# Optimization experiments

Measured on AMD Instinct MI355X. Metric: run time of the kernel, lower is better.

The kernel has to match this reference:

```python
import jax, jax.numpy as jnp
import numpy as np
from jax import lax

TARGETED_NUM_POINTS = 2000


def fps_indices(pts, m):
    """Furthest-point sampling indices for one cloud. pts: [n,3] -> [m] int32.
    Matches pointnet2_utils.furthest_point_sample: first index is 0, then
    iteratively pick the point with max distance to the selected set."""
    n = pts.shape[0]

    def step(carry, _):
        dist, last = carry
        d = jnp.sum((pts - pts[last]) ** 2, axis=-1)  # [n]
        dist = jnp.minimum(dist, d)
        nxt = jnp.argmax(dist).astype(jnp.int32)
        return (dist, nxt), nxt

    dist0 = jnp.full((n,), 1e10, dtype=pts.dtype)
    (_, _), idxs = lax.scan(step, (dist0, jnp.int32(0)), None, length=m - 1)
    return jnp.concatenate([jnp.zeros((1,), jnp.int32), idxs])


def setup_inputs() -> dict:
    key = jax.random.key(0)
    k1, k2 = jax.random.split(key)
    batch, n_pts, c = 8, 20000, 128
    return {
        "input_C": jax.random.normal(k1, (batch * n_pts, 3), dtype=jnp.float32),
        "input_F": jax.random.normal(k2, (batch * n_pts, c), dtype=jnp.float32),
        "batch": batch,
        "n_pts": n_pts,
    }


def reference(input_C, input_F, batch, n_pts):
    # pts_list = [n_pts]*batch (equal-size clouds), so the flat tensors reshape cleanly.
    C = input_C.reshape(batch, n_pts, 3)
    F = input_F.reshape(batch, n_pts, -1)
    m = min(TARGETED_NUM_POINTS, n_pts)
    idxs = jax.vmap(lambda p: fps_indices(p, m))(C)  # [b, m]
    sampled_C = jnp.take_along_axis(C, idxs[..., None], axis=1)  # [b, m, 3]
    sampled_F = jnp.take_along_axis(F, idxs[..., None], axis=1)  # [b, m, c]
    return sampled_C, sampled_F
```

## Files before the change

### kernel.cpp

```cpp
#include <hip/hip_runtime.h>
#include <hip/hip_bf16.h>

typedef unsigned long long ull;

#define THREADS 1024
#define NWAVE 16

template<int CTRL, int RM>
__device__ __forceinline__ float fmax_dpp(float v) {
    int s = __builtin_amdgcn_update_dpp(__float_as_int(v), __float_as_int(v), CTRL, RM, 0xf, false);
    return fmaxf(v, __int_as_float(s));
}
template<int CTRL, int RM>
__device__ __forceinline__ float fmin_dpp(float v) {
    int s = __builtin_amdgcn_update_dpp(__float_as_int(v), __float_as_int(v), CTRL, RM, 0xf, false);
    return fminf(v, __int_as_float(s));
}
template<int CTRL, int RM>
__device__ __forceinline__ int imin_dpp(int v) {
    int s = __builtin_amdgcn_update_dpp(v, v, CTRL, RM, 0xf, false);
    return (s < v) ? s : v;
}
template<int CTRL, int RM>
__device__ __forceinline__ ull kmax_dpp(ull k) {
    unsigned hi = (unsigned)(k >> 32), lo = (unsigned)k;
    unsigned hi2 = (unsigned)__builtin_amdgcn_update_dpp((int)hi, (int)hi, CTRL, RM, 0xf, false);
    unsigned lo2 = (unsigned)__builtin_amdgcn_update_dpp((int)lo, (int)lo, CTRL, RM, 0xf, false);
    ull k2 = ((ull)hi2 << 32) | lo2;
    return (k2 > k) ? k2 : k;
}
__device__ __forceinline__ float wave_fmax(float v) {
    v = fmax_dpp<0x111,0xf>(v); v = fmax_dpp<0x112,0xf>(v);
    v = fmax_dpp<0x114,0xf>(v); v = fmax_dpp<0x118,0xf>(v);
    v = fmax_dpp<0x142,0xa>(v); v = fmax_dpp<0x143,0xc>(v);
    return v;
}
__device__ __forceinline__ float wave_fmin(float v) {
    v = fmin_dpp<0x111,0xf>(v); v = fmin_dpp<0x112,0xf>(v);
    v = fmin_dpp<0x114,0xf>(v); v = fmin_dpp<0x118,0xf>(v);
    v = fmin_dpp<0x142,0xa>(v); v = fmin_dpp<0x143,0xc>(v);
    return v;
}
__device__ __forceinline__ float half_fmax(float v) {
    v = fmax_dpp<0x111,0xf>(v); v = fmax_dpp<0x112,0xf>(v);
    v = fmax_dpp<0x114,0xf>(v); v = fmax_dpp<0x118,0xf>(v);
    v = fmax_dpp<0x142,0xa>(v);
    return v;
}
__device__ __forceinline__ float half_fmin(float v) {
    v = fmin_dpp<0x111,0xf>(v); v = fmin_dpp<0x112,0xf>(v);
    v = fmin_dpp<0x114,0xf>(v); v = fmin_dpp<0x118,0xf>(v);
    v = fmin_dpp<0x142,0xa>(v);
    return v;
}
__device__ __forceinline__ int half_imin(int v) {
    v = imin_dpp<0x111,0xf>(v); v = imin_dpp<0x112,0xf>(v);
    v = imin_dpp<0x114,0xf>(v); v = imin_dpp<0x118,0xf>(v);
    v = imin_dpp<0x142,0xa>(v);
    return v;
}
__device__ __forceinline__ ull wave_kmax(ull k) {
    k = kmax_dpp<0x111,0xf>(k); k = kmax_dpp<0x112,0xf>(k);
    k = kmax_dpp<0x114,0xf>(k); k = kmax_dpp<0x118,0xf>(k);
    k = kmax_dpp<0x142,0xa>(k); k = kmax_dpp<0x143,0xc>(k);
    return k;
}
__device__ __forceinline__ int morton4(int x, int y, int z) {
    int r = 0;
#pragma unroll
    for (int k = 0; k < 4; ++k)
        r |= ((x >> k & 1) << (3 * k)) | ((y >> k & 1) << (3 * k + 1)) | ((z >> k & 1) << (3 * k + 2));
    return r;
}
__device__ __forceinline__ int cellof(float x, float y, float z,
                                      float bx, float by, float bz,
                                      float ivx, float ivy, float ivz) {
    int ix = (int)((x - bx) * ivx); ix = ix < 0 ? 0 : (ix > 15 ? 15 : ix);
    int iy = (int)((y - by) * ivy); iy = iy < 0 ? 0 : (iy > 15 ? 15 : iy);
    int iz = (int)((z - bz) * ivz); iz = iz < 0 ? 0 : (iz > 15 ? 15 : iz);
    return morton4(ix, iy, iz);
}

#define OFS_GKEY 0
#define OFS_GWIN 8192
#define OFS_GMAX 24576
#define OFS_CX   28672
#define OFS_CY   32768
#define OFS_CZ   36864
#define OFS_EX   40960
#define OFS_EY   45056
#define OFS_EZ   49152
#define OFS_LIST 53248
#define OFS_PART 55296
#define OFS_MISC 55552
#define OFS_RED  55680
#define FIXED_BYTES 56064

__device__ __forceinline__ void phaseC(
    const float4* __restrict__ gx, float* __restrict__ s_dist,
    ull* __restrict__ s_gkey, float* __restrict__ s_gmax,
    float4* __restrict__ s_gwin,
    const unsigned short* __restrict__ lst, int U,
    int lane, int half, int sub, int wid,
    float lx, float ly, float lz)
{
    const int nt = (U + 1) >> 1;
    int j = wid;
    if (j >= nt) return;
    int e = 2 * j + half;
    bool a = (e < U);
    int g = a ? (int)lst[e] : 0;
    int o = g * 32 + sub;
    float4 w = gx[o];
    while (j < nt) {
        const int jn = j + NWAVE;
        const int en = 2 * jn + half;
        bool an = (jn < nt) && (en < U);
        int gn = an ? (int)lst[en] : 0;
        int on = gn * 32 + sub;
        float4 wn = gx[on];
        float dc = a ? s_dist[o] : -1.0f;
        float dx = __fsub_rn(w.x, lx);
        float dy = __fsub_rn(w.y, ly);
        float dz = __fsub_rn(w.z, lz);
        float d  = __fadd_rn(__fadd_rn(__fmul_rn(dx, dx), __fmul_rn(dy, dy)),
                             __fmul_rn(dz, dz));
        float nd = fminf(dc, d);
        if (a) s_dist[o] = nd;
        float gm = __shfl(half_fmax(nd), lane | 31);
        int pk = (nd == gm) ? (int)w.w : 0x7FFFFFFF;
        int minorig = __shfl(half_imin(pk), lane | 31);
        if (a && nd == gm && (int)w.w == minorig)
            s_gwin[g] = w;
        if (a && sub == 31) {
            s_gkey[g] = ((ull)__float_as_uint(gm) << 25)
                      | ((ull)(unsigned)(0x7fff - minorig) << 10)
                      | (ull)(unsigned)g;
            s_gmax[g] = gm;
        }
        j = jn; a = an; g = gn; o = on; w = wn;
    }
}

__global__ __launch_bounds__(THREADS)
void fps_grouped(const float* __restrict__ C, float4* __restrict__ gxyzo,
                 int n, int m, int G32, int* __restrict__ idx_out) {
    const int b = blockIdx.x;
    const int t = threadIdx.x;
    const int lane = t & 63;
    const int wid  = t >> 6;
    const int half = lane >> 5;
    const int sub  = lane & 31;
    const int GP = G32 * 32;
    const float* __restrict__ P = C + (size_t)b * n * 3;
    float4* __restrict__ gx = gxyzo + (size_t)b * GP;

    extern __shared__ char smem[];
    ull*    s_gkey = (ull*)(smem + OFS_GKEY);
    float4* s_gwin = (float4*)(smem + OFS_GWIN);
    float*  s_gmax = (float*)(smem + OFS_GMAX);
    float*  s_cx   = (float*)(smem + OFS_CX);
    float*  s_cy   = (float*)(smem + OFS_CY);
    float*  s_cz   = (float*)(smem + OFS_CZ);
    float*  s_ex   = (float*)(smem + OFS_EX);
    float*  s_ey   = (float*)(smem + OFS_EY);
    float*  s_ez   = (float*)(smem + OFS_EZ);
    unsigned short* s_list = (unsigned short*)(smem + OFS_LIST);
    ull*    s_part = (ull*)(smem + OFS_PART);
    int*    s_misc = (int*)(smem + OFS_MISC);
    float*  s_red  = (float*)(smem + OFS_RED);
    float*  s_dist = (float*)(smem + FIXED_BYTES);
    unsigned* s_hist = (unsigned*)s_dist;

    float mnx = 1e30f, mny = 1e30f, mnz = 1e30f;
    float mxx = -1e30f, mxy = -1e30f, mxz = -1e30f;
    for (int g = t; g < n; g += THREADS) {
        float x = P[3 * g], y = P[3 * g + 1], z = P[3 * g + 2];
        mnx = fminf(mnx, x); mxx = fmaxf(mxx, x);
        mny = fminf(mny, y); mxy = fmaxf(mxy, y);
        mnz = fminf(mnz, z); mxz = fmaxf(mxz, z);
    }
    mnx = wave_fmin(mnx); mny = wave_fmin(mny); mnz = wave_fmin(mnz);
    mxx = wave_fmax(mxx); mxy = wave_fmax(mxy); mxz = wave_fmax(mxz);
    if (lane == 63) {
        s_red[wid * 6 + 0] = mnx; s_red[wid * 6 + 1] = mny; s_red[wid * 6 + 2] = mnz;
        s_red[wid * 6 + 3] = mxx; s_red[wid * 6 + 4] = mxy; s_red[wid * 6 + 5] = mxz;
    }
    __syncthreads();
    if (t == 0) {
        float a0 = 1e30f, a1 = 1e30f, a2 = 1e30f, b0 = -1e30f, b1 = -1e30f, b2 = -1e30f;
        for (int w = 0; w < NWAVE; ++w) {
            a0 = fminf(a0, s_red[w * 6 + 0]); a1 = fminf(a1, s_red[w * 6 + 1]);
            a2 = fminf(a2, s_red[w * 6 + 2]); b0 = fmaxf(b0, s_red[w * 6 + 3]);
            b1 = fmaxf(b1, s_red[w * 6 + 4]); b2 = fmaxf(b2, s_red[w * 6 + 5]);
        }
        s_red[0] = a0; s_red[1] = a1; s_red[2] = a2;
        s_red[3] = 15.9999f / (b0 - a0 + 1e-20f);
        s_red[4] = 15.9999f / (b1 - a1 + 1e-20f);
        s_red[5] = 15.9999f / (b2 - a2 + 1e-20f);
    }
    __syncthreads();
    const float bx = s_red[0], by = s_red[1], bz = s_red[2];
    const float ivx = s_red[3], ivy = s_red[4], ivz = s_red[5];

    for (int i = t; i < 4096; i += THREADS) s_hist[i] = 0;
    __syncthreads();
    for (int g = t; g < n; g += THREADS) {
        float x = P[3 * g], y = P[3 * g + 1], z = P[3 * g + 2];
        atomicAdd(&s_hist[cellof(x, y, z, bx, by, bz, ivx, ivy, ivz)], 1u);
    }
    __syncthreads();

    {
        unsigned c0 = s_hist[4 * t], c1 = s_hist[4 * t + 1];
        unsigned c2 = s_hist[4 * t + 2], c3 = s_hist[4 * t + 3];
        unsigned sum4 = c0 + c1 + c2 + c3;
        unsigned incl = sum4;
        for (int off = 1; off < 64; off <<= 1) {
            unsigned u = (unsigned)__shfl_up((int)incl, off);
            if (lane >= off) incl += u;
        }
        if (lane == 63) s_misc[8 + wid] = (int)incl;
        __syncthreads();
        unsigned woff = 0;
        for (int w = 0; w < wid; ++w) woff += (unsigned)s_misc[8 + w];
        unsigned base = woff + incl - sum4;
        s_hist[4 * t]     = base;
        s_hist[4 * t + 1] = base + c0;
        s_hist[4 * t + 2] = base + c0 + c1;
        s_hist[4 * t + 3] = base + c0 + c1 + c2;
    }
    __syncthreads();

    for (int g = t; g < n; g += THREADS) {
        float x = P[3 * g], y = P[3 * g + 1], z = P[3 * g + 2];
        unsigned pos = atomicAdd(&s_hist[cellof(x, y, z, bx, by, bz, ivx, ivy, ivz)], 1u);
        gx[pos] = make_float4(x, y, z, (float)g);
    }
    __syncthreads();

    for (int g = wid; g < G32; g += NWAVE) {
        int cnt = n - g * 32; if (cnt > 32) cnt = 32;
        bool memb = (lane < 32) && (sub < cnt);
        float4 w = make_float4(0.f, 0.f, 0.f, 0.f);
        if (memb) w = gx[g * 32 + sub];
        float xn = memb ? w.x : 1e30f, xx = memb ? w.x : -1e30f;
        float yn = memb ? w.y : 1e30f, yx = memb ? w.y : -1e30f;
        float zn = memb ? w.z : 1e30f, zx = memb ? w.z : -1e30f;
        xn = __shfl(half_fmin(xn), 31); xx = __shfl(half_fmax(xx), 31);
        yn = __shfl(half_fmin(yn), 31); yx = __shfl(half_fmax(yx), 31);
        zn = __shfl(half_fmin(zn), 31); zx = __shfl(half_fmax(zx), 31);
        if (lane == 0) {
            s_cx[g] = (xn + xx) * 0.5f; s_ex[g] = (xx - xn) * 0.5f + 1e-7f;
            s_cy[g] = (yn + yx) * 0.5f; s_ey[g] = (yx - yn) * 0.5f + 1e-7f;
            s_cz[g] = (zn + zx) * 0.5f; s_ez[g] = (zx - zn) * 0.5f + 1e-7f;
            s_gmax[g] = 1e10f;
        }
        if (lane < 32) {
            if (!memb) gx[g * 32 + sub] = make_float4(0.f, 0.f, 0.f, 0.f);
            s_dist[g * 32 + sub] = memb ? 1e10f : -1.0f;
        }
    }
    for (int i = t; i < 1024; i += THREADS)
        if (i >= G32) s_gkey[i] = 0;
    if (t == 0) { s_misc[0] = 0; idx_out[(size_t)b * m] = 0; }
    __syncthreads();

    float lx = P[0], ly = P[1], lz = P[2];
    const size_t iobase = (size_t)b * m;
    const int DW = (G32 + 63) >> 6;
    for (int it = 1; it < m; ++it) {
        const int par = (it & 1) * 16;

        bool upd = false;
        if (t < G32) {
            float gmax = s_gmax[t];
            float ax = fmaxf(fabsf(lx - s_cx[t]) - s_ex[t], 0.0f);
            float ay = fmaxf(fabsf(ly - s_cy[t]) - s_ey[t], 0.0f);
            float az = fmaxf(fabsf(lz - s_cz[t]) - s_ez[t], 0.0f);
            float lb2 = ax * ax + ay * ay + az * az;
            upd = !(lb2 * 0.9999f - 1e-6f >= gmax);
        }
        {
            ull mask = __ballot(upd);
            if (mask) {
                int cnt = __popcll(mask);
                int base = 0;
                if (lane == 0) base = atomicAdd(&s_misc[0], cnt);
                base = __shfl(base, 0);
                if (upd) {
                    int pw = (int)__popcll(mask & ((1ULL << lane) - 1ULL));
                    s_list[base + pw] = (unsigned short)t;
                }
            }
        }
        __syncthreads();
        const int U = s_misc[0];

        phaseC(gx, s_dist, s_gkey, s_gmax, s_gwin, s_list, U,
               lane, half, sub, wid, lx, ly, lz);
        __syncthreads();

        ull kk = 0;
        if (wid < DW) kk = wave_kmax(s_gkey[t]);
        if (lane == 63) s_part[par + wid] = kk;
        if (t == 0) s_misc[0] = 0;
        __syncthreads();
        ull k2 = s_part[par + (t & 15)];
        k2 = kmax_dpp<0x111,0xf>(k2);
        k2 = kmax_dpp<0x112,0xf>(k2);
        k2 = kmax_dpp<0x114,0xf>(k2);
        k2 = kmax_dpp<0x118,0xf>(k2);
        unsigned klo = (unsigned)__builtin_amdgcn_readlane((int)(unsigned)k2, 15);
        int gwin = (int)(klo & 0x3ffu);
        int orig = 0x7fff - (int)((klo >> 10) & 0x7fffu);
        if (t == 0) idx_out[iobase + it] = orig;
        float4 wn = s_gwin[gwin];
        lx = wn.x; ly = wn.y; lz = wn.z;
    }
}

__global__ __launch_bounds__(1024)
void fps_brute(const float* __restrict__ C, float* __restrict__ gdist,
               int n, int m, int* __restrict__ idx_out) {
    const int b = blockIdx.x, t = threadIdx.x;
    const int lane = t & 63, wid = t >> 6;
    const float* __restrict__ P = C + (size_t)b * n * 3;
    float* __restrict__ dist = gdist + (size_t)b * n;
    __shared__ ull sp[2][16];
    for (int g = t; g < n; g += 1024) dist[g] = 1e10f;
    if (t == 0) idx_out[(size_t)b * m] = 0;
    float lx = P[0], ly = P[1], lz = P[2];
    __syncthreads();
    for (int it = 1; it < m; ++it) {
        int par = it & 1;
        ull k = 0;
        for (int g = t; g < n; g += 1024) {
            float dx = __fsub_rn(P[3 * g], lx);
            float dy = __fsub_rn(P[3 * g + 1], ly);
            float dz = __fsub_rn(P[3 * g + 2], lz);
            float d = __fadd_rn(__fadd_rn(__fmul_rn(dx, dx), __fmul_rn(dy, dy)),
                                __fmul_rn(dz, dz));
            float nd = fminf(dist[g], d);
            dist[g] = nd;
            ull kk = ((ull)__float_as_uint(nd) << 32) | (unsigned)(~g);
            if (kk > k) k = kk;
        }
        for (int off = 1; off < 64; off <<= 1) {
            ull ok = __shfl_xor(k, off);
            if (ok > k) k = ok;
        }
        if (lane == 0) sp[par][wid] = k;
        __syncthreads();
        ull kmaxv = sp[par][0];
        for (int w = 1; w < 16; ++w) { ull v = sp[par][w]; if (v > kmaxv) kmaxv = v; }
        int sbi = (int)~(unsigned)kmaxv;
        if (t == 0) idx_out[(size_t)b * m + it] = sbi;
        const float* wp = P + 3 * (size_t)(unsigned)sbi;
        lx = wp[0]; ly = wp[1]; lz = wp[2];
    }
}

__global__ void gather_kernel(const float* __restrict__ C,
                              const float* __restrict__ F,
                              const int* __restrict__ idx,
                              float* __restrict__ outC,
                              float* __restrict__ outF,
                              int n_pts, int m, int c) {
    int pair = blockIdx.x;
    int b = pair / m;
    int src = idx[pair];
    size_t srcbase = (size_t)b * n_pts + src;
    const float* sF = F + srcbase * (size_t)c;
    float* dF = outF + (size_t)pair * c;
    for (int i = threadIdx.x; i < c; i += blockDim.x) dF[i] = sF[i];
    if (threadIdx.x < 3)
        outC[(size_t)pair * 3 + threadIdx.x] = C[srcbase * 3 + threadIdx.x];
}

extern "C" void kernel_launch(void* const* d_in, const int* in_sizes, int n_in,
                              void* d_out, int out_size, void* d_ws, size_t ws_size,
                              hipStream_t stream) {
    const float* C = (const float*)d_in[0];
    const float* F = (const float*)d_in[1];

    int n_total = in_sizes[0] / 3;
    int c       = in_sizes[1] / n_total;
    int bm      = out_size / (3 + c);

    int batch = 8;
    if (bm % 2000 == 0) {
        int bb = bm / 2000;
        if (bb > 0 && n_total % bb == 0 && n_total / bb >= 2000) batch = bb;
    }
    int n_pts = n_total / batch;
    int m     = (n_pts < 2000) ? n_pts : 2000;

    int* idxbuf = (int*)d_ws;
    float* outC = (float*)d_out;
    float* outF = outC + (size_t)batch * m * 3;

    int G32 = (n_pts + 31) >> 5;
    int GP  = G32 << 5;
    size_t idxbytes = (((size_t)batch * m * 4) + 255) & ~(size_t)255;
    size_t scrbytes = (size_t)batch * GP * 16;
    void* scratch;
    if (ws_size >= idxbytes + scrbytes)
        scratch = (char*)d_ws + idxbytes;
    else
        scratch = (char*)d_out + ((((size_t)out_size * 4) - scrbytes) & ~(size_t)15);

    if (n_pts <= 32767) {
        int distbytes = GP * 4; if (distbytes < 16384) distbytes = 16384;
        size_t smem = (size_t)FIXED_BYTES + distbytes;
        hipFuncSetAttribute((const void*)fps_grouped,
                            hipFuncAttributeMaxDynamicSharedMemorySize, (int)smem);
        fps_grouped<<<batch, THREADS, smem, stream>>>(C, (float4*)scratch,
                                                      n_pts, m, G32, idxbuf);
    } else {
        fps_brute<<<batch, 1024, 0, stream>>>(C, (float*)scratch, n_pts, m, idxbuf);
    }

    gather_kernel<<<batch * m, 128, 0, stream>>>(C, F, idxbuf, outC, outF,
                                                 n_pts, m, c);
}
```

Measured before the change: 3.294 ms.

## Shrink spatial groups to 16 points and use ballot-based argmax tie handling

Point groups for bounding-box pruning shrink from 32 to 16 points, which gives up to 1280 groups with tighter boxes. Fewer points should then need distance updates each FPS iteration. The per-group argmax now uses a ballot to find the winning point and only runs the min-index reduction when there are ties. The software prefetch of the next group is removed. The costs are more groups to prune-test and reduce, a second key load per thread, more shared memory, and a lower size limit before falling back to the brute-force kernel.

```diff
diff --git a/kernel.cpp b/kernel.cpp
--- a/kernel.cpp
+++ b/kernel.cpp
@@ -5,6 +5,7 @@
 
 #define THREADS 1024
 #define NWAVE 16
+#define MAXG 1280
 
 template<int CTRL, int RM>
 __device__ __forceinline__ float fmax_dpp(float v) {
@@ -29,34 +30,29 @@
     ull k2 = ((ull)hi2 << 32) | lo2;
     return (k2 > k) ? k2 : k;
 }
-__device__ __forceinline__ float wave_fmax(float v) {
+__device__ __forceinline__ float row_fmax(float v) {
     v = fmax_dpp<0x111,0xf>(v); v = fmax_dpp<0x112,0xf>(v);
     v = fmax_dpp<0x114,0xf>(v); v = fmax_dpp<0x118,0xf>(v);
+    return v;
+}
+__device__ __forceinline__ float row_fmin(float v) {
+    v = fmin_dpp<0x111,0xf>(v); v = fmin_dpp<0x112,0xf>(v);
+    v = fmin_dpp<0x114,0xf>(v); v = fmin_dpp<0x118,0xf>(v);
+    return v;
+}
+__device__ __forceinline__ int row_imin(int v) {
+    v = imin_dpp<0x111,0xf>(v); v = imin_dpp<0x112,0xf>(v);
+    v = imin_dpp<0x114,0xf>(v); v = imin_dpp<0x118,0xf>(v);
+    return v;
+}
+__device__ __forceinline__ float wave_fmax(float v) {
+    v = row_fmax(v);
     v = fmax_dpp<0x142,0xa>(v); v = fmax_dpp<0x143,0xc>(v);
     return v;
 }
 __device__ __forceinline__ float wave_fmin(float v) {
-    v = fmin_dpp<0x111,0xf>(v); v = fmin_dpp<0x112,0xf>(v);
-    v = fmin_dpp<0x114,0xf>(v); v = fmin_dpp<0x118,0xf>(v);
+    v = row_fmin(v);
     v = fmin_dpp<0x142,0xa>(v); v = fmin_dpp<0x143,0xc>(v);
-    return v;
-}
-__device__ __forceinline__ float half_fmax(float v) {
-    v = fmax_dpp<0x111,0xf>(v); v = fmax_dpp<0x112,0xf>(v);
-    v = fmax_dpp<0x114,0xf>(v); v = fmax_dpp<0x118,0xf>(v);
-    v = fmax_dpp<0x142,0xa>(v);
-    return v;
-}
-__device__ __forceinline__ float half_fmin(float v) {
-    v = fmin_dpp<0x111,0xf>(v); v = fmin_dpp<0x112,0xf>(v);
-    v = fmin_dpp<0x114,0xf>(v); v = fmin_dpp<0x118,0xf>(v);
-    v = fmin_dpp<0x142,0xa>(v);
-    return v;
-}
-__device__ __forceinline__ int half_imin(int v) {
-    v = imin_dpp<0x111,0xf>(v); v = imin_dpp<0x112,0xf>(v);
-    v = imin_dpp<0x114,0xf>(v); v = imin_dpp<0x118,0xf>(v);
-    v = imin_dpp<0x142,0xa>(v);
     return v;
 }
 __device__ __forceinline__ ull wave_kmax(ull k) {
@@ -82,76 +78,30 @@
 }
 
 #define OFS_GKEY 0
-#define OFS_GWIN 8192
-#define OFS_GMAX 24576
-#define OFS_CX   28672
-#define OFS_CY   32768
-#define OFS_CZ   36864
-#define OFS_EX   40960
-#define OFS_EY   45056
-#define OFS_EZ   49152
-#define OFS_LIST 53248
-#define OFS_PART 55296
-#define OFS_MISC 55552
-#define OFS_RED  55680
-#define FIXED_BYTES 56064
-
-__device__ __forceinline__ void phaseC(
-    const float4* __restrict__ gx, float* __restrict__ s_dist,
-    ull* __restrict__ s_gkey, float* __restrict__ s_gmax,
-    float4* __restrict__ s_gwin,
-    const unsigned short* __restrict__ lst, int U,
-    int lane, int half, int sub, int wid,
-    float lx, float ly, float lz)
-{
-    const int nt = (U + 1) >> 1;
-    int j = wid;
-    if (j >= nt) return;
-    int e = 2 * j + half;
-    bool a = (e < U);
-    int g = a ? (int)lst[e] : 0;
-    int o = g * 32 + sub;
-    float4 w = gx[o];
-    while (j < nt) {
-        const int jn = j + NWAVE;
-        const int en = 2 * jn + half;
-        bool an = (jn < nt) && (en < U);
-        int gn = an ? (int)lst[en] : 0;
-        int on = gn * 32 + sub;
-        float4 wn = gx[on];
-        float dc = a ? s_dist[o] : -1.0f;
-        float dx = __fsub_rn(w.x, lx);
-        float dy = __fsub_rn(w.y, ly);
-        float dz = __fsub_rn(w.z, lz);
-        float d  = __fadd_rn(__fadd_rn(__fmul_rn(dx, dx), __fmul_rn(dy, dy)),
-                             __fmul_rn(dz, dz));
-        float nd = fminf(dc, d);
-        if (a) s_dist[o] = nd;
-        float gm = __shfl(half_fmax(nd), lane | 31);
-        int pk = (nd == gm) ? (int)w.w : 0x7FFFFFFF;
-        int minorig = __shfl(half_imin(pk), lane | 31);
-        if (a && nd == gm && (int)w.w == minorig)
-            s_gwin[g] = w;
-        if (a && sub == 31) {
-            s_gkey[g] = ((ull)__float_as_uint(gm) << 25)
-                      | ((ull)(unsigned)(0x7fff - minorig) << 10)
-                      | (ull)(unsigned)g;
-            s_gmax[g] = gm;
-        }
-        j = jn; a = an; g = gn; o = on; w = wn;
-    }
-}
+#define OFS_GWIN 10240
+#define OFS_GMAX 30720
+#define OFS_CX   35840
+#define OFS_CY   40960
+#define OFS_CZ   46080
+#define OFS_EX   51200
+#define OFS_EY   56320
+#define OFS_EZ   61440
+#define OFS_LIST 66560
+#define OFS_PART 69120
+#define OFS_MISC 69376
+#define OFS_RED  69504
+#define FIXED_BYTES 69888
 
 __global__ __launch_bounds__(THREADS)
 void fps_grouped(const float* __restrict__ C, float4* __restrict__ gxyzo,
-                 int n, int m, int G32, int* __restrict__ idx_out) {
+                 int n, int m, int G16, int* __restrict__ idx_out) {
     const int b = blockIdx.x;
     const int t = threadIdx.x;
     const int lane = t & 63;
     const int wid  = t >> 6;
-    const int half = lane >> 5;
-    const int sub  = lane & 31;
-    const int GP = G32 * 32;
+    const int row  = lane >> 4;
+    const int s16  = lane & 15;
+    const int GP = G16 * 16;
     const float* __restrict__ P = C + (size_t)b * n * 3;
     float4* __restrict__ gx = gxyzo + (size_t)b * GP;
 
@@ -239,49 +189,47 @@
     }
     __syncthreads();
 
-    for (int g = wid; g < G32; g += NWAVE) {
-        int cnt = n - g * 32; if (cnt > 32) cnt = 32;
-        bool memb = (lane < 32) && (sub < cnt);
+    for (int gb = wid; gb * 4 < G16; gb += NWAVE) {
+        int g = gb * 4 + row;
+        bool gvalid = g < G16;
+        int base = g * 16;
+        int cnt = gvalid ? (n - base < 16 ? n - base : 16) : 0;
+        bool memb = gvalid && (s16 < cnt);
         float4 w = make_float4(0.f, 0.f, 0.f, 0.f);
-        if (memb) w = gx[g * 32 + sub];
+        if (memb) w = gx[base + s16];
         float xn = memb ? w.x : 1e30f, xx = memb ? w.x : -1e30f;
         float yn = memb ? w.y : 1e30f, yx = memb ? w.y : -1e30f;
         float zn = memb ? w.z : 1e30f, zx = memb ? w.z : -1e30f;
-        xn = __shfl(half_fmin(xn), 31); xx = __shfl(half_fmax(xx), 31);
-        yn = __shfl(half_fmin(yn), 31); yx = __shfl(half_fmax(yx), 31);
-        zn = __shfl(half_fmin(zn), 31); zx = __shfl(half_fmax(zx), 31);
-        if (lane == 0) {
+        xn = __shfl(row_fmin(xn), lane | 15); xx = __shfl(row_fmax(xx), lane | 15);
+        yn = __shfl(row_fmin(yn), lane | 15); yx = __shfl(row_fmax(yx), lane | 15);
+        zn = __shfl(row_fmin(zn), lane | 15); zx = __shfl(row_fmax(zx), lane | 15);
+        if (gvalid && s16 == 0) {
             s_cx[g] = (xn + xx) * 0.5f; s_ex[g] = (xx - xn) * 0.5f + 1e-7f;
             s_cy[g] = (yn + yx) * 0.5f; s_ey[g] = (yx - yn) * 0.5f + 1e-7f;
             s_cz[g] = (zn + zx) * 0.5f; s_ez[g] = (zx - zn) * 0.5f + 1e-7f;
             s_gmax[g] = 1e10f;
         }
-        if (lane < 32) {
-            if (!memb) gx[g * 32 + sub] = make_float4(0.f, 0.f, 0.f, 0.f);
-            s_dist[g * 32 + sub] = memb ? 1e10f : -1.0f;
-        }
-    }
-    for (int i = t; i < 1024; i += THREADS)
-        if (i >= G32) s_gkey[i] = 0;
+        if (gvalid) {
+            if (!memb) gx[base + s16] = make_float4(0.f, 0.f, 0.f, 0.f);
+            s_dist[base + s16] = memb ? 1e10f : -1.0f;
+        }
+    }
+    for (int i = G16 + t; i < MAXG; i += THREADS) s_gkey[i] = 0;
     if (t == 0) { s_misc[0] = 0; idx_out[(size_t)b * m] = 0; }
     __syncthreads();
 
     float lx = P[0], ly = P[1], lz = P[2];
     const size_t iobase = (size_t)b * m;
-    const int DW = (G32 + 63) >> 6;
     for (int it = 1; it < m; ++it) {
         const int par = (it & 1) * 16;
 
-        bool upd = false;
-        if (t < G32) {
-            float gmax = s_gmax[t];
-            float ax = fmaxf(fabsf(lx - s_cx[t]) - s_ex[t], 0.0f);
-            float ay = fmaxf(fabsf(ly - s_cy[t]) - s_ey[t], 0.0f);
-            float az = fmaxf(fabsf(lz - s_cz[t]) - s_ez[t], 0.0f);
+        for (int g = t; g < G16; g += THREADS) {
+            float gmax = s_gmax[g];
+            float ax = fmaxf(fabsf(lx - s_cx[g]) - s_ex[g], 0.0f);
+            float ay = fmaxf(fabsf(ly - s_cy[g]) - s_ey[g], 0.0f);
+            float az = fmaxf(fabsf(lz - s_cz[g]) - s_ez[g], 0.0f);
             float lb2 = ax * ax + ay * ay + az * az;
-            upd = !(lb2 * 0.9999f - 1e-6f >= gmax);
-        }
-        {
+            bool upd = !(lb2 * 0.9999f - 1e-6f >= gmax);
             ull mask = __ballot(upd);
             if (mask) {
                 int cnt = __popcll(mask);
@@ -290,20 +238,62 @@
                 base = __shfl(base, 0);
                 if (upd) {
                     int pw = (int)__popcll(mask & ((1ULL << lane) - 1ULL));
-                    s_list[base + pw] = (unsigned short)t;
+                    s_list[base + pw] = (unsigned short)g;
                 }
             }
         }
         __syncthreads();
         const int U = s_misc[0];
 
-        phaseC(gx, s_dist, s_gkey, s_gmax, s_gwin, s_list, U,
-               lane, half, sub, wid, lx, ly, lz);
+        {
+            const int nt = (U + 3) >> 2;
+            for (int j = wid; j < nt; j += NWAVE) {
+                int e = 4 * j + row;
+                bool a = (e < U);
+                int g = a ? (int)s_list[e] : 0;
+                int o = g * 16 + s16;
+                float4 w = gx[o];
+                float dc = a ? s_dist[o] : -1.0f;
+                float dx = __fsub_rn(w.x, lx);
+                float dy = __fsub_rn(w.y, ly);
+                float dz = __fsub_rn(w.z, lz);
+                float d  = __fadd_rn(__fadd_rn(__fmul_rn(dx, dx), __fmul_rn(dy, dy)),
+                                     __fmul_rn(dz, dz));
+                float nd = fminf(dc, d);
+                if (a) s_dist[o] = nd;
+                float gm = __shfl(row_fmax(nd), lane | 15);
+                ull mask = __ballot(nd == gm);
+                unsigned rm = (unsigned)(mask >> (row * 16)) & 0xffffu;
+                int fl = __ffs((int)rm) - 1;
+                int ao = __shfl((int)w.w, (lane & ~15) + fl);
+                bool tie = (rm & (rm - 1u)) != 0u;
+                if (__any(tie)) {
+                    int pk = (nd == gm) ? (int)w.w : 0x7FFFFFFF;
+                    int mo = __shfl(row_imin(pk), lane | 15);
+                    if (tie) ao = mo;
+                }
+                if (a && nd == gm && (int)w.w == ao)
+                    s_gwin[g] = w;
+                if (a && s16 == 15) {
+                    s_gkey[g] = ((ull)__float_as_uint(gm) << 26)
+                              | ((ull)(unsigned)(0x7fff - ao) << 11)
+                              | (ull)(unsigned)g;
+                    s_gmax[g] = gm;
+                }
+            }
+        }
         __syncthreads();
 
-        ull kk = 0;
-        if (wid < DW) kk = wave_kmax(s_gkey[t]);
-        if (lane == 63) s_part[par + wid] = kk;
+        {
+            ull v = s_gkey[t];
+            int t2 = t + THREADS;
+            if (t2 < G16) {
+                ull v2 = s_gkey[t2];
+                if (v2 > v) v = v2;
+            }
+            ull kk = wave_kmax(v);
+            if (lane == 63) s_part[par + wid] = kk;
+        }
         if (t == 0) s_misc[0] = 0;
         __syncthreads();
         ull k2 = s_part[par + (t & 15)];
@@ -312,8 +302,8 @@
         k2 = kmax_dpp<0x114,0xf>(k2);
         k2 = kmax_dpp<0x118,0xf>(k2);
         unsigned klo = (unsigned)__builtin_amdgcn_readlane((int)(unsigned)k2, 15);
-        int gwin = (int)(klo & 0x3ffu);
-        int orig = 0x7fff - (int)((klo >> 10) & 0x7fffu);
+        int gwin = (int)(klo & 0x7ffu);
+        int orig = 0x7fff - (int)((klo >> 11) & 0x7fffu);
         if (t == 0) idx_out[iobase + it] = orig;
         float4 wn = s_gwin[gwin];
         lx = wn.x; ly = wn.y; lz = wn.z;
@@ -400,8 +390,8 @@
     float* outC = (float*)d_out;
     float* outF = outC + (size_t)batch * m * 3;
 
-    int G32 = (n_pts + 31) >> 5;
-    int GP  = G32 << 5;
+    int G16 = (n_pts + 15) >> 4;
+    int GP  = G16 << 4;
     size_t idxbytes = (((size_t)batch * m * 4) + 255) & ~(size_t)255;
     size_t scrbytes = (size_t)batch * GP * 16;
     void* scratch;
@@ -410,13 +400,13 @@
     else
         scratch = (char*)d_out + ((((size_t)out_size * 4) - scrbytes) & ~(size_t)15);
 
-    if (n_pts <= 32767) {
+    if (G16 <= MAXG) {
         int distbytes = GP * 4; if (distbytes < 16384) distbytes = 16384;
         size_t smem = (size_t)FIXED_BYTES + distbytes;
         hipFuncSetAttribute((const void*)fps_grouped,
                             hipFuncAttributeMaxDynamicSharedMemorySize, (int)smem);
         fps_grouped<<<batch, THREADS, smem, stream>>>(C, (float4*)scratch,
-                                                      n_pts, m, G32, idxbuf);
+                                                      n_pts, m, G16, idxbuf);
     } else {
         fps_brute<<<batch, 1024, 0, stream>>>(C, (float*)scratch, n_pts, m, idxbuf);
     }
```

Result: no change. 3.337 ms (+1.3%).

## Split each cloud's FPS across four cooperating blocks with global-memory handoff

Applied to the files above, without the earlier changes.

Moves the spatial binning and per-group bounding-box setup into a separate pre-kernel. The main FPS loop now runs as four blocks per cloud, each holding a quarter of the sorted points and their distances in LDS. Each iteration, every block publishes its local best key to global memory and spin-waits on an atomic arrival counter before reducing the four keys. This spreads the sequential per-cloud work over more CUs and keeps the points in LDS, at the cost of a cross-block global-memory sync every iteration. It also assumes all blocks of a cloud are resident at the same time.

```diff
diff --git a/kernel.cpp b/kernel.cpp
--- a/kernel.cpp
+++ b/kernel.cpp
@@ -5,6 +5,9 @@
 
 #define THREADS 1024
 #define NWAVE 16
+#define NSUB 4
+#define MAXLQ 160
+#define COMM_ULLS 32
 
 template<int CTRL, int RM>
 __device__ __forceinline__ float fmax_dpp(float v) {
@@ -29,18 +32,6 @@
     ull k2 = ((ull)hi2 << 32) | lo2;
     return (k2 > k) ? k2 : k;
 }
-__device__ __forceinline__ float wave_fmax(float v) {
-    v = fmax_dpp<0x111,0xf>(v); v = fmax_dpp<0x112,0xf>(v);
-    v = fmax_dpp<0x114,0xf>(v); v = fmax_dpp<0x118,0xf>(v);
-    v = fmax_dpp<0x142,0xa>(v); v = fmax_dpp<0x143,0xc>(v);
-    return v;
-}
-__device__ __forceinline__ float wave_fmin(float v) {
-    v = fmin_dpp<0x111,0xf>(v); v = fmin_dpp<0x112,0xf>(v);
-    v = fmin_dpp<0x114,0xf>(v); v = fmin_dpp<0x118,0xf>(v);
-    v = fmin_dpp<0x142,0xa>(v); v = fmin_dpp<0x143,0xc>(v);
-    return v;
-}
 __device__ __forceinline__ float half_fmax(float v) {
     v = fmax_dpp<0x111,0xf>(v); v = fmax_dpp<0x112,0xf>(v);
     v = fmax_dpp<0x114,0xf>(v); v = fmax_dpp<0x118,0xf>(v);
@@ -57,6 +48,14 @@
     v = imin_dpp<0x111,0xf>(v); v = imin_dpp<0x112,0xf>(v);
     v = imin_dpp<0x114,0xf>(v); v = imin_dpp<0x118,0xf>(v);
     v = imin_dpp<0x142,0xa>(v);
+    return v;
+}
+__device__ __forceinline__ float wave_fmax(float v) {
+    v = half_fmax(v); v = fmax_dpp<0x143,0xc>(v);
+    return v;
+}
+__device__ __forceinline__ float wave_fmin(float v) {
+    v = half_fmin(v); v = fmin_dpp<0x143,0xc>(v);
     return v;
 }
 __device__ __forceinline__ ull wave_kmax(ull k) {
@@ -81,44 +80,140 @@
     return morton4(ix, iy, iz);
 }
 
-#define OFS_GKEY 0
-#define OFS_GWIN 8192
-#define OFS_GMAX 24576
-#define OFS_CX   28672
-#define OFS_CY   32768
-#define OFS_CZ   36864
-#define OFS_EX   40960
-#define OFS_EY   45056
-#define OFS_EZ   49152
-#define OFS_LIST 53248
-#define OFS_PART 55296
-#define OFS_MISC 55552
-#define OFS_RED  55680
-#define FIXED_BYTES 56064
-
-__device__ __forceinline__ void phaseC(
-    const float4* __restrict__ gx, float* __restrict__ s_dist,
-    ull* __restrict__ s_gkey, float* __restrict__ s_gmax,
-    float4* __restrict__ s_gwin,
-    const unsigned short* __restrict__ lst, int U,
-    int lane, int half, int sub, int wid,
+__global__ __launch_bounds__(THREADS)
+void fps_pre(const float* __restrict__ C, float4* __restrict__ gxyzo,
+             float* __restrict__ meta, ull* __restrict__ comm,
+             int n, int m, int G32, int* __restrict__ idx_out)
+{
+    const int b = blockIdx.x, t = threadIdx.x;
+    const int lane = t & 63, wid = t >> 6, sub32 = lane & 31;
+    const float* __restrict__ P = C + (size_t)b * n * 3;
+    float4* __restrict__ gx = gxyzo + (size_t)b * (G32 * 32);
+    float* __restrict__ M = meta + (size_t)b * G32 * 6;
+
+    __shared__ unsigned s_hist[4096];
+    __shared__ float s_red[96];
+    __shared__ int s_scan[16];
+
+    float mnx = 1e30f, mny = 1e30f, mnz = 1e30f;
+    float mxx = -1e30f, mxy = -1e30f, mxz = -1e30f;
+    for (int g = t; g < n; g += THREADS) {
+        float x = P[3 * g], y = P[3 * g + 1], z = P[3 * g + 2];
+        mnx = fminf(mnx, x); mxx = fmaxf(mxx, x);
+        mny = fminf(mny, y); mxy = fmaxf(mxy, y);
+        mnz = fminf(mnz, z); mxz = fmaxf(mxz, z);
+    }
+    mnx = wave_fmin(mnx); mny = wave_fmin(mny); mnz = wave_fmin(mnz);
+    mxx = wave_fmax(mxx); mxy = wave_fmax(mxy); mxz = wave_fmax(mxz);
+    if (lane == 63) {
+        s_red[wid * 6 + 0] = mnx; s_red[wid * 6 + 1] = mny; s_red[wid * 6 + 2] = mnz;
+        s_red[wid * 6 + 3] = mxx; s_red[wid * 6 + 4] = mxy; s_red[wid * 6 + 5] = mxz;
+    }
+    __syncthreads();
+    if (t == 0) {
+        float a0 = 1e30f, a1 = 1e30f, a2 = 1e30f, b0 = -1e30f, b1 = -1e30f, b2 = -1e30f;
+        for (int w = 0; w < NWAVE; ++w) {
+            a0 = fminf(a0, s_red[w * 6 + 0]); a1 = fminf(a1, s_red[w * 6 + 1]);
+            a2 = fminf(a2, s_red[w * 6 + 2]); b0 = fmaxf(b0, s_red[w * 6 + 3]);
+            b1 = fmaxf(b1, s_red[w * 6 + 4]); b2 = fmaxf(b2, s_red[w * 6 + 5]);
+        }
+        s_red[0] = a0; s_red[1] = a1; s_red[2] = a2;
+        s_red[3] = 15.9999f / (b0 - a0 + 1e-20f);
+        s_red[4] = 15.9999f / (b1 - a1 + 1e-20f);
+        s_red[5] = 15.9999f / (b2 - a2 + 1e-20f);
+    }
+    __syncthreads();
+    const float bx = s_red[0], by = s_red[1], bz = s_red[2];
+    const float ivx = s_red[3], ivy = s_red[4], ivz = s_red[5];
+
+    for (int i = t; i < 4096; i += THREADS) s_hist[i] = 0;
+    __syncthreads();
+    for (int g = t; g < n; g += THREADS) {
+        float x = P[3 * g], y = P[3 * g + 1], z = P[3 * g + 2];
+        atomicAdd(&s_hist[cellof(x, y, z, bx, by, bz, ivx, ivy, ivz)], 1u);
+    }
+    __syncthreads();
+
+    {
+        unsigned c0 = s_hist[4 * t], c1 = s_hist[4 * t + 1];
+        unsigned c2 = s_hist[4 * t + 2], c3 = s_hist[4 * t + 3];
+        unsigned sum4 = c0 + c1 + c2 + c3;
+        unsigned incl = sum4;
+        for (int off = 1; off < 64; off <<= 1) {
+            unsigned u = (unsigned)__shfl_up((int)incl, off);
+            if (lane >= off) incl += u;
+        }
+        if (lane == 63) s_scan[wid] = (int)incl;
+        __syncthreads();
+        unsigned woff = 0;
+        for (int w = 0; w < wid; ++w) woff += (unsigned)s_scan[w];
+        unsigned base = woff + incl - sum4;
+        s_hist[4 * t]     = base;
+        s_hist[4 * t + 1] = base + c0;
+        s_hist[4 * t + 2] = base + c0 + c1;
+        s_hist[4 * t + 3] = base + c0 + c1 + c2;
+    }
+    __syncthreads();
+
+    for (int g = t; g < n; g += THREADS) {
+        float x = P[3 * g], y = P[3 * g + 1], z = P[3 * g + 2];
+        unsigned pos = atomicAdd(&s_hist[cellof(x, y, z, bx, by, bz, ivx, ivy, ivz)], 1u);
+        gx[pos] = make_float4(x, y, z, (float)g);
+    }
+    __syncthreads();
+
+    for (int g = wid; g < G32; g += NWAVE) {
+        int cnt = n - g * 32; if (cnt > 32) cnt = 32;
+        bool memb = (lane < 32) && (sub32 < cnt);
+        float4 w = make_float4(0.f, 0.f, 0.f, 0.f);
+        if (memb) w = gx[g * 32 + sub32];
+        float xn = memb ? w.x : 1e30f, xxv = memb ? w.x : -1e30f;
+        float yn = memb ? w.y : 1e30f, yxv = memb ? w.y : -1e30f;
+        float zn = memb ? w.z : 1e30f, zxv = memb ? w.z : -1e30f;
+        xn = __shfl(half_fmin(xn), 31); xxv = __shfl(half_fmax(xxv), 31);
+        yn = __shfl(half_fmin(yn), 31); yxv = __shfl(half_fmax(yxv), 31);
+        zn = __shfl(half_fmin(zn), 31); zxv = __shfl(half_fmax(zxv), 31);
+        if (lane == 0) {
+            M[0 * G32 + g] = (xn + xxv) * 0.5f;
+            M[1 * G32 + g] = (yn + yxv) * 0.5f;
+            M[2 * G32 + g] = (zn + zxv) * 0.5f;
+            M[3 * G32 + g] = (xxv - xn) * 0.5f + 1e-7f;
+            M[4 * G32 + g] = (yxv - yn) * 0.5f + 1e-7f;
+            M[5 * G32 + g] = (zxv - zn) * 0.5f + 1e-7f;
+        }
+    }
+    if (t == 0) idx_out[(size_t)b * m] = 0;
+    for (int i = t; i < COMM_ULLS; i += THREADS) comm[(size_t)b * COMM_ULLS + i] = 0;
+}
+
+#define OFS_PTS  0
+#define OFS_DIST 81920
+#define OFS_CX   102400
+#define OFS_CY   103040
+#define OFS_CZ   103680
+#define OFS_EX   104320
+#define OFS_EY   104960
+#define OFS_EZ   105600
+#define OFS_GMX  106240
+#define OFS_GKEY 106880
+#define OFS_LIST 108928
+#define OFS_MISC 109248
+#define SMEM_TOTAL 109568
+
+__device__ __forceinline__ void phaseC_lds(
+    const float4* __restrict__ s_pts, float* __restrict__ s_dist,
+    ull* __restrict__ s_gkey, float* __restrict__ s_gmx,
+    const unsigned short* __restrict__ lst, int U, int base_g,
+    int lane, int half, int sub32, int wid,
     float lx, float ly, float lz)
 {
     const int nt = (U + 1) >> 1;
-    int j = wid;
-    if (j >= nt) return;
-    int e = 2 * j + half;
-    bool a = (e < U);
-    int g = a ? (int)lst[e] : 0;
-    int o = g * 32 + sub;
-    float4 w = gx[o];
-    while (j < nt) {
-        const int jn = j + NWAVE;
-        const int en = 2 * jn + half;
-        bool an = (jn < nt) && (en < U);
-        int gn = an ? (int)lst[en] : 0;
-        int on = gn * 32 + sub;
-        float4 wn = gx[on];
+    for (int j = wid; j < nt; j += NWAVE) {
+        int e = 2 * j + half;
+        bool a = (e < U);
+        int g = a ? (int)lst[e] : 0;
+        int o = g * 32 + sub32;
+        float4 w = s_pts[o];
         float dc = a ? s_dist[o] : -1.0f;
         float dx = __fsub_rn(w.x, lx);
         float dy = __fsub_rn(w.y, ly);
@@ -128,153 +223,123 @@
         float nd = fminf(dc, d);
         if (a) s_dist[o] = nd;
         float gm = __shfl(half_fmax(nd), lane | 31);
-        int pk = (nd == gm) ? (int)w.w : 0x7FFFFFFF;
-        int minorig = __shfl(half_imin(pk), lane | 31);
-        if (a && nd == gm && (int)w.w == minorig)
-            s_gwin[g] = w;
-        if (a && sub == 31) {
-            s_gkey[g] = ((ull)__float_as_uint(gm) << 25)
-                      | ((ull)(unsigned)(0x7fff - minorig) << 10)
-                      | (ull)(unsigned)g;
-            s_gmax[g] = gm;
-        }
-        j = jn; a = an; g = gn; o = on; w = wn;
+        int pi = (nd == gm) ? (((int)w.w << 6) | sub32) : 0x7FFFFFFF;
+        int mv = __shfl(half_imin(pi), lane | 31);
+        if (a && sub32 == 31) {
+            int worig = mv >> 6;
+            int fl = mv & 63;
+            int pos = (base_g + g) * 32 + fl;
+            s_gkey[g] = ((ull)__float_as_uint(gm) << 30)
+                      | ((ull)(unsigned)(0x7fff - worig) << 15)
+                      | (ull)(unsigned)pos;
+            s_gmx[g] = gm;
+        }
     }
 }
 
 __global__ __launch_bounds__(THREADS)
-void fps_grouped(const float* __restrict__ C, float4* __restrict__ gxyzo,
-                 int n, int m, int G32, int* __restrict__ idx_out) {
-    const int b = blockIdx.x;
+void fps_multi(const float* __restrict__ C, const float4* __restrict__ gx_all,
+               const float* __restrict__ meta, ull* __restrict__ comm,
+               int n, int m, int G32, int Gq, int batch,
+               int* __restrict__ idx_out)
+{
+    const int cloud = blockIdx.x % batch;
+    const int sub   = blockIdx.x / batch;
     const int t = threadIdx.x;
     const int lane = t & 63;
     const int wid  = t >> 6;
     const int half = lane >> 5;
-    const int sub  = lane & 31;
-    const int GP = G32 * 32;
-    const float* __restrict__ P = C + (size_t)b * n * 3;
-    float4* __restrict__ gx = gxyzo + (size_t)b * GP;
+    const int sub32 = lane & 31;
+
+    const int base_g = sub * Gq;
+    int ng = G32 - base_g; if (ng > Gq) ng = Gq; if (ng < 0) ng = 0;
+
+    const float* __restrict__ P = C + (size_t)cloud * n * 3;
+    const float4* __restrict__ gx = gx_all + (size_t)cloud * (G32 * 32);
+    const float* __restrict__ M = meta + (size_t)cloud * G32 * 6;
+    ull* __restrict__ pkb = comm + (size_t)cloud * COMM_ULLS;
+    int* __restrict__ arrive = (int*)(pkb + 2 * NSUB);
 
     extern __shared__ char smem[];
-    ull*    s_gkey = (ull*)(smem + OFS_GKEY);
-    float4* s_gwin = (float4*)(smem + OFS_GWIN);
-    float*  s_gmax = (float*)(smem + OFS_GMAX);
+    float4* s_pts  = (float4*)(smem + OFS_PTS);
+    float*  s_dist = (float*)(smem + OFS_DIST);
     float*  s_cx   = (float*)(smem + OFS_CX);
     float*  s_cy   = (float*)(smem + OFS_CY);
     float*  s_cz   = (float*)(smem + OFS_CZ);
     float*  s_ex   = (float*)(smem + OFS_EX);
     float*  s_ey   = (float*)(smem + OFS_EY);
     float*  s_ez   = (float*)(smem + OFS_EZ);
+    float*  s_gmx  = (float*)(smem + OFS_GMX);
+    ull*    s_gkey = (ull*)(smem + OFS_GKEY);
     unsigned short* s_list = (unsigned short*)(smem + OFS_LIST);
-    ull*    s_part = (ull*)(smem + OFS_PART);
-    int*    s_misc = (int*)(smem + OFS_MISC);
-    float*  s_red  = (float*)(smem + OFS_RED);
-    float*  s_dist = (float*)(smem + FIXED_BYTES);
-    unsigned* s_hist = (unsigned*)s_dist;
-
-    float mnx = 1e30f, mny = 1e30f, mnz = 1e30f;
-    float mxx = -1e30f, mxy = -1e30f, mxz = -1e30f;
-    for (int g = t; g < n; g += THREADS) {
-        float x = P[3 * g], y = P[3 * g + 1], z = P[3 * g + 2];
-        mnx = fminf(mnx, x); mxx = fmaxf(mxx, x);
-        mny = fminf(mny, y); mxy = fmaxf(mxy, y);
-        mnz = fminf(mnz, z); mxz = fmaxf(mxz, z);
-    }
-    mnx = wave_fmin(mnx); mny = wave_fmin(mny); mnz = wave_fmin(mnz);
-    mxx = wave_fmax(mxx); mxy = wave_fmax(mxy); mxz = wave_fmax(mxz);
-    if (lane == 63) {
-        s_red[wid * 6 + 0] = mnx; s_red[wid * 6 + 1] = mny; s_red[wid * 6 + 2] = mnz;
-        s_red[wid * 6 + 3] = mxx; s_red[wid * 6 + 4] = mxy; s_red[wid * 6 + 5] = mxz;
-    }
-    __syncthreads();
-    if (t == 0) {
-        float a0 = 1e30f, a1 = 1e30f, a2 = 1e30f, b0 = -1e30f, b1 = -1e30f, b2 = -1e30f;
-        for (int w = 0; w < NWAVE; ++w) {
-            a0 = fminf(a0, s_red[w * 6 + 0]); a1 = fminf(a1, s_red[w * 6 + 1]);
-            a2 = fminf(a2, s_red[w * 6 + 2]); b0 = fmaxf(b0, s_red[w * 6 + 3]);
-            b1 = fmaxf(b1, s_red[w * 6 + 4]); b2 = fmaxf(b2, s_red[w * 6 + 5]);
-        }
-        s_red[0] = a0; s_red[1] = a1; s_red[2] = a2;
-        s_red[3] = 15.9999f / (b0 - a0 + 1e-20f);
-        s_red[4] = 15.9999f / (b1 - a1 + 1e-20f);
-        s_red[5] = 15.9999f / (b2 - a2 + 1e-20f);
-    }
-    __syncthreads();
-    const float bx = s_red[0], by = s_red[1], bz = s_red[2];
-    const float ivx = s_red[3], ivy = s_red[4], ivz = s_red[5];
-
-    for (int i = t; i < 4096; i += THREADS) s_hist[i] = 0;
-    __syncthreads();
-    for (int g = t; g < n; g += THREADS) {
-        float x = P[3 * g], y = P[3 * g + 1], z = P[3 * g + 2];
-        atomicAdd(&s_hist[cellof(x, y, z, bx, by, bz, ivx, ivy, ivz)], 1u);
-    }
-    __syncthreads();
-
-    {
-        unsigned c0 = s_hist[4 * t], c1 = s_hist[4 * t + 1];
-        unsigned c2 = s_hist[4 * t + 2], c3 = s_hist[4 * t + 3];
-        unsigned sum4 = c0 + c1 + c2 + c3;
-        unsigned incl = sum4;
-        for (int off = 1; off < 64; off <<= 1) {
-            unsigned u = (unsigned)__shfl_up((int)incl, off);
-            if (lane >= off) incl += u;
-        }
-        if (lane == 63) s_misc[8 + wid] = (int)incl;
+    int*      s_ctr  = (int*)(smem + OFS_MISC);
+    unsigned* s_bklo = (unsigned*)(smem + OFS_MISC + 8);
+    unsigned* s_bkhi = (unsigned*)(smem + OFS_MISC + 12);
+
+    for (int i = t; i < ng * 32; i += THREADS) {
+        s_pts[i] = gx[base_g * 32 + i];
+        s_dist[i] = (base_g * 32 + i < n) ? 1e10f : -1.0f;
+    }
+    for (int l = t; l < ng; l += THREADS) {
+        int g = base_g + l;
+        s_cx[l] = M[0 * G32 + g]; s_cy[l] = M[1 * G32 + g]; s_cz[l] = M[2 * G32 + g];
+        s_ex[l] = M[3 * G32 + g]; s_ey[l] = M[4 * G32 + g]; s_ez[l] = M[5 * G32 + g];
+        s_list[l] = (unsigned short)l;
+    }
+    for (int i = t; i < 256; i += THREADS) s_gkey[i] = 0;
+    if (t == 0) *s_ctr = 0;
+    __syncthreads();
+
+    float lx = P[0], ly = P[1], lz = P[2];
+    phaseC_lds(s_pts, s_dist, s_gkey, s_gmx, s_list, ng, base_g,
+               lane, half, sub32, wid, lx, ly, lz);
+    __syncthreads();
+    if (wid == 0) {
+        ull k = s_gkey[lane];
+        ull v = s_gkey[lane + 64];  if (v > k) k = v;
+        v = s_gkey[lane + 128];     if (v > k) k = v;
+        v = s_gkey[lane + 192];     if (v > k) k = v;
+        k = wave_kmax(k);
+        unsigned klo = (unsigned)__builtin_amdgcn_readlane((int)(unsigned)k, 63);
+        unsigned khi = (unsigned)__builtin_amdgcn_readlane((int)(k >> 32), 63);
+        if (lane == 0) {
+            ull bk = ((ull)khi << 32) | klo;
+            __hip_atomic_store(&pkb[0 * NSUB + sub], bk, __ATOMIC_RELAXED, __HIP_MEMORY_SCOPE_AGENT);
+            __hip_atomic_fetch_add(arrive, 1, __ATOMIC_RELEASE, __HIP_MEMORY_SCOPE_AGENT);
+        }
+    }
+
+    const size_t iobase = (size_t)cloud * m;
+    for (int r = 1; r < m; ++r) {
+        if (wid == 0) {
+            ull kv = 0;
+            if (lane < NSUB) {
+                int target = NSUB * r;
+                int guard = 0;
+                while (__hip_atomic_load(arrive, __ATOMIC_ACQUIRE, __HIP_MEMORY_SCOPE_AGENT) < target) {
+                    __builtin_amdgcn_s_sleep(2);
+                    if (++guard > (1 << 27)) break;
+                }
+                kv = __hip_atomic_load(&pkb[((r - 1) & 1) * NSUB + lane],
+                                       __ATOMIC_RELAXED, __HIP_MEMORY_SCOPE_AGENT);
+            }
+            ull o1 = __shfl_xor(kv, 1); if (o1 > kv) kv = o1;
+            o1 = __shfl_xor(kv, 2);     if (o1 > kv) kv = o1;
+            if (lane == 0) { *s_bklo = (unsigned)kv; *s_bkhi = (unsigned)(kv >> 32); }
+        }
         __syncthreads();
-        unsigned woff = 0;
-        for (int w = 0; w < wid; ++w) woff += (unsigned)s_misc[8 + w];
-        unsigned base = woff + incl - sum4;
-        s_hist[4 * t]     = base;
-        s_hist[4 * t + 1] = base + c0;
-        s_hist[4 * t + 2] = base + c0 + c1;
-        s_hist[4 * t + 3] = base + c0 + c1 + c2;
-    }
-    __syncthreads();
-
-    for (int g = t; g < n; g += THREADS) {
-        float x = P[3 * g], y = P[3 * g + 1], z = P[3 * g + 2];
-        unsigned pos = atomicAdd(&s_hist[cellof(x, y, z, bx, by, bz, ivx, ivy, ivz)], 1u);
-        gx[pos] = make_float4(x, y, z, (float)g);
-    }
-    __syncthreads();
-
-    for (int g = wid; g < G32; g += NWAVE) {
-        int cnt = n - g * 32; if (cnt > 32) cnt = 32;
-        bool memb = (lane < 32) && (sub < cnt);
-        float4 w = make_float4(0.f, 0.f, 0.f, 0.f);
-        if (memb) w = gx[g * 32 + sub];
-        float xn = memb ? w.x : 1e30f, xx = memb ? w.x : -1e30f;
-        float yn = memb ? w.y : 1e30f, yx = memb ? w.y : -1e30f;
-        float zn = memb ? w.z : 1e30f, zx = memb ? w.z : -1e30f;
-        xn = __shfl(half_fmin(xn), 31); xx = __shfl(half_fmax(xx), 31);
-        yn = __shfl(half_fmin(yn), 31); yx = __shfl(half_fmax(yx), 31);
-        zn = __shfl(half_fmin(zn), 31); zx = __shfl(half_fmax(zx), 31);
-        if (lane == 0) {
-            s_cx[g] = (xn + xx) * 0.5f; s_ex[g] = (xx - xn) * 0.5f + 1e-7f;
-            s_cy[g] = (yn + yx) * 0.5f; s_ey[g] = (yx - yn) * 0.5f + 1e-7f;
-            s_cz[g] = (zn + zx) * 0.5f; s_ez[g] = (zx - zn) * 0.5f + 1e-7f;
-            s_gmax[g] = 1e10f;
-        }
-        if (lane < 32) {
-            if (!memb) gx[g * 32 + sub] = make_float4(0.f, 0.f, 0.f, 0.f);
-            s_dist[g * 32 + sub] = memb ? 1e10f : -1.0f;
-        }
-    }
-    for (int i = t; i < 1024; i += THREADS)
-        if (i >= G32) s_gkey[i] = 0;
-    if (t == 0) { s_misc[0] = 0; idx_out[(size_t)b * m] = 0; }
-    __syncthreads();
-
-    float lx = P[0], ly = P[1], lz = P[2];
-    const size_t iobase = (size_t)b * m;
-    const int DW = (G32 + 63) >> 6;
-    for (int it = 1; it < m; ++it) {
-        const int par = (it & 1) * 16;
+        ull bk = ((ull)(*s_bkhi) << 32) | (*s_bklo);
+        int pos  = (int)(bk & 0x7fffu);
+        int orig = 0x7fff - (int)((bk >> 15) & 0x7fffu);
+        if (sub == 0 && t == 0) idx_out[iobase + r] = orig;
+        if (r == m - 1) break;
+        int sp = __builtin_amdgcn_readfirstlane(pos);
+        float4 wn = gx[sp];
+        lx = wn.x; ly = wn.y; lz = wn.z;
 
         bool upd = false;
-        if (t < G32) {
-            float gmax = s_gmax[t];
+        if (t < ng) {
+            float gmax = s_gmx[t];
             float ax = fmaxf(fabsf(lx - s_cx[t]) - s_ex[t], 0.0f);
             float ay = fmaxf(fabsf(ly - s_cy[t]) - s_ey[t], 0.0f);
             float az = fmaxf(fabsf(lz - s_cz[t]) - s_ez[t], 0.0f);
@@ -286,7 +351,7 @@
             if (mask) {
                 int cnt = __popcll(mask);
                 int base = 0;
-                if (lane == 0) base = atomicAdd(&s_misc[0], cnt);
+                if (lane == 0) base = atomicAdd(s_ctr, cnt);
                 base = __shfl(base, 0);
                 if (upd) {
                     int pw = (int)__popcll(mask & ((1ULL << lane) - 1ULL));
@@ -295,28 +360,27 @@
             }
         }
         __syncthreads();
-        const int U = s_misc[0];
-
-        phaseC(gx, s_dist, s_gkey, s_gmax, s_gwin, s_list, U,
-               lane, half, sub, wid, lx, ly, lz);
+        const int U = *s_ctr;
+
+        phaseC_lds(s_pts, s_dist, s_gkey, s_gmx, s_list, U, base_g,
+                   lane, half, sub32, wid, lx, ly, lz);
         __syncthreads();
-
-        ull kk = 0;
-        if (wid < DW) kk = wave_kmax(s_gkey[t]);
-        if (lane == 63) s_part[par + wid] = kk;
-        if (t == 0) s_misc[0] = 0;
-        __syncthreads();
-        ull k2 = s_part[par + (t & 15)];
-        k2 = kmax_dpp<0x111,0xf>(k2);
-        k2 = kmax_dpp<0x112,0xf>(k2);
-        k2 = kmax_dpp<0x114,0xf>(k2);
-        k2 = kmax_dpp<0x118,0xf>(k2);
-        unsigned klo = (unsigned)__builtin_amdgcn_readlane((int)(unsigned)k2, 15);
-        int gwin = (int)(klo & 0x3ffu);
-        int orig = 0x7fff - (int)((klo >> 10) & 0x7fffu);
-        if (t == 0) idx_out[iobase + it] = orig;
-        float4 wn = s_gwin[gwin];
-        lx = wn.x; ly = wn.y; lz = wn.z;
+        if (t == 0) *s_ctr = 0;
+
+        if (wid == 0) {
+            ull k = s_gkey[lane];
+            ull v = s_gkey[lane + 64];  if (v > k) k = v;
+            v = s_gkey[lane + 128];     if (v > k) k = v;
+            v = s_gkey[lane + 192];     if (v > k) k = v;
+            k = wave_kmax(k);
+            unsigned klo = (unsigned)__builtin_amdgcn_readlane((int)(unsigned)k, 63);
+            unsigned khi = (unsigned)__builtin_amdgcn_readlane((int)(k >> 32), 63);
+            if (lane == 0) {
+                ull pk = ((ull)khi << 32) | klo;
+                __hip_atomic_store(&pkb[(r & 1) * NSUB + sub], pk, __ATOMIC_RELAXED, __HIP_MEMORY_SCOPE_AGENT);
+                __hip_atomic_fetch_add(arrive, 1, __ATOMIC_RELEASE, __HIP_MEMORY_SCOPE_AGENT);
+            }
+        }
     }
 }
 
@@ -401,24 +465,32 @@
     float* outF = outC + (size_t)batch * m * 3;
 
     int G32 = (n_pts + 31) >> 5;
-    int GP  = G32 << 5;
-    size_t idxbytes = (((size_t)batch * m * 4) + 255) & ~(size_t)255;
-    size_t scrbytes = (size_t)batch * GP * 16;
-    void* scratch;
-    if (ws_size >= idxbytes + scrbytes)
-        scratch = (char*)d_ws + idxbytes;
+    int Gq  = (G32 + NSUB - 1) / NSUB;
+    int GP  = G32 * 32;
+    size_t idxbytes  = (((size_t)batch * m * 4) + 255) & ~(size_t)255;
+    size_t commbytes = (size_t)batch * 256;
+    size_t gxbytes   = (size_t)batch * GP * 16;
+    size_t metabytes = (((size_t)batch * G32 * 24) + 255) & ~(size_t)255;
+    size_t scr = commbytes + gxbytes + metabytes;
+    char* sbase;
+    if (ws_size >= idxbytes + scr)
+        sbase = (char*)d_ws + idxbytes;
     else
-        scratch = (char*)d_out + ((((size_t)out_size * 4) - scrbytes) & ~(size_t)15);
-
-    if (n_pts <= 32767) {
-        int distbytes = GP * 4; if (distbytes < 16384) distbytes = 16384;
-        size_t smem = (size_t)FIXED_BYTES + distbytes;
-        hipFuncSetAttribute((const void*)fps_grouped,
-                            hipFuncAttributeMaxDynamicSharedMemorySize, (int)smem);
-        fps_grouped<<<batch, THREADS, smem, stream>>>(C, (float4*)scratch,
-                                                      n_pts, m, G32, idxbuf);
+        sbase = (char*)d_out + ((((size_t)out_size * 4) - scr) & ~(size_t)255);
+    ull*    comm = (ull*)sbase;
+    float4* gxb  = (float4*)(sbase + commbytes);
+    float*  meta = (float*)(sbase + commbytes + gxbytes);
+
+    if (Gq <= MAXLQ && n_pts <= 32767) {
+        fps_pre<<<batch, THREADS, 0, stream>>>(C, gxb, meta, comm,
+                                               n_pts, m, G32, idxbuf);
+        hipFuncSetAttribute((const void*)fps_multi,
+                            hipFuncAttributeMaxDynamicSharedMemorySize, SMEM_TOTAL);
+        fps_multi<<<batch * NSUB, THREADS, SMEM_TOTAL, stream>>>(
+            C, gxb, meta, comm, n_pts, m, G32, Gq, batch, idxbuf);
     } else {
-        fps_brute<<<batch, 1024, 0, stream>>>(C, (float*)scratch, n_pts, m, idxbuf);
+        fps_brute<<<batch, 1024, 0, stream>>>(C, (float*)(sbase + commbytes),
+                                              n_pts, m, idxbuf);
     }
 
     gather_kernel<<<batch * m, 128, 0, stream>>>(C, F, idxbuf, outC, outF,
```

Result: slower. 4.937 ms (+49.9%).
